# Performance work log

Measured on AMD Instinct MI355X. Metric: run time of the kernel, lower is better.

## Reference

```python
import jax, jax.numpy as jnp
import numpy as np
from jax import lax

B, DIM, H, W = 4, 192, 128, 128
NUM_HEADS = 4
EPS = 1e-12


def _conv1x1(x, w):
    # x: [b,c,h,w], w: [o,i,1,1]
    return lax.conv_general_dilated(x, w, (1, 1), 'VALID',
                                    dimension_numbers=('NCHW', 'OIHW', 'NCHW'))


def _dwconv3x3(x, w):
    # depthwise: w: [c,1,3,3], groups = c
    return lax.conv_general_dilated(x, w, (1, 1), ((1, 1), (1, 1)),
                                    dimension_numbers=('NCHW', 'OIHW', 'NCHW'),
                                    feature_group_count=w.shape[0])


def _l2norm(t):
    # normalize along last (spatial) axis, torch F.normalize semantics
    n = jnp.sqrt(jnp.sum(t * t, axis=-1, keepdims=True))
    return t / jnp.maximum(n, EPS)


def _heads(t, b, h, w):
    # [b, head*c, h, w] -> [b, head, c, h*w]
    return t.reshape(b, NUM_HEADS, t.shape[1] // NUM_HEADS, h * w)


def setup_inputs() -> dict:
    key = jax.random.key(0)
    ks = jax.random.split(key, 9)
    s = 0.02
    return {
        'x': jax.random.normal(ks[0], (B, DIM, H, W), jnp.float32),
        'ctx': jax.random.normal(ks[1], (B, DIM, H, W), jnp.float32),
        'x_qkv_w': jax.random.normal(ks[2], (DIM * 3, DIM, 1, 1), jnp.float32) * s,
        'x_dw_w': jax.random.normal(ks[3], (DIM * 3, 1, 3, 3), jnp.float32) * s,
        'x_po_w': jax.random.normal(ks[4], (DIM, DIM, 1, 1), jnp.float32) * s,
        'ctx_qkv_w': jax.random.normal(ks[5], (DIM * 3, DIM, 1, 1), jnp.float32) * s,
        'ctx_dw_w': jax.random.normal(ks[6], (DIM * 3, 1, 3, 3), jnp.float32) * s,
        'ctx_po_w': jax.random.normal(ks[7], (DIM, DIM, 1, 1), jnp.float32) * s,
        'temperature': jnp.ones((NUM_HEADS, 1, 1), jnp.float32),
    }


def reference(x, ctx, x_qkv_w, x_dw_w, x_po_w, ctx_qkv_w, ctx_dw_w, ctx_po_w, temperature):
    b, c, h, w = x.shape
    x_qkv = _dwconv3x3(_conv1x1(x, x_qkv_w), x_dw_w)
    x_q, x_k, x_v = jnp.split(x_qkv, 3, axis=1)
    ctx_qkv = _dwconv3x3(_conv1x1(ctx, ctx_qkv_w), ctx_dw_w)
    ctx_q, ctx_k, ctx_v = jnp.split(ctx_qkv, 3, axis=1)

    x_q, x_k, x_v = (_heads(t, b, h, w) for t in (x_q, x_k, x_v))
    ctx_q, ctx_k, ctx_v = (_heads(t, b, h, w) for t in (ctx_q, ctx_k, ctx_v))

    temp = temperature[None]  # [1, head, 1, 1]

    # ctx branch: x_q attends over ctx
    q1 = _l2norm(x_q)
    k1 = _l2norm(ctx_k)
    attn1 = jax.nn.softmax(jnp.einsum('bhcn,bhdn->bhcd', q1, k1) * temp, axis=-1)
    ctx_out = jnp.einsum('bhcd,bhdn->bhcn', attn1, ctx_v).reshape(b, c, h, w)
    ctx_out = _conv1x1(ctx_out, ctx_po_w)

    # x branch: ctx_q attends over x
    q2 = _l2norm(ctx_q)
    k2 = _l2norm(x_k)
    attn2 = jax.nn.softmax(jnp.einsum('bhcn,bhdn->bhcd', q2, k2) * temp, axis=-1)
    x_out = jnp.einsum('bhcd,bhdn->bhcn', attn2, x_v).reshape(b, c, h, w)
    x_out = _conv1x1(x_out, x_po_w)

    return (x_out, ctx_out)
```

## Files before the change

### kernel.cpp

```cpp
#include <hip/hip_runtime.h>
#include <hip/hip_bf16.h>

#define N_PIX 16384
#define W_ 128

typedef __attribute__((ext_vector_type(8))) unsigned short ushort8_t;
typedef __attribute__((ext_vector_type(4))) unsigned short ushort4_t;
typedef __attribute__((ext_vector_type(8))) __bf16 bf16x8;
typedef __attribute__((ext_vector_type(4))) float f32x4;

__device__ inline float bf2f(unsigned short u) {
    return __uint_as_float(((unsigned)u) << 16);
}
__device__ inline unsigned short f2bf(float f) {
    __hip_bfloat16 h = __float2bfloat16(f);
    return *(unsigned short*)&h;
}

__global__ __launch_bounds__(256) void k_pack_w(
    const float* __restrict__ wa, const float* __restrict__ wb,
    unsigned short* __restrict__ oa, unsigned short* __restrict__ ob)
{
    const int blk = blockIdx.x;
    const float* w = (blk < 108) ? wa : wb;
    unsigned short* o = (blk < 108) ? oa : ob;
    const int i = ((blk % 108) * 256 + threadIdx.x) * 4;
    float4 v = *(const float4*)(w + i);
    ushort4_t s;
    s[0] = f2bf(v.x); s[1] = f2bf(v.y); s[2] = f2bf(v.z); s[3] = f2bf(v.w);
    *(ushort4_t*)(o + i) = s;
}

__global__ __launch_bounds__(256, 2) void k_conv_mfma(
    const float* __restrict__ x, const float* __restrict__ ctx,
    const unsigned short* __restrict__ wx, const unsigned short* __restrict__ wc,
    unsigned short* __restrict__ ox, unsigned short* __restrict__ octx)
{
    const int p0 = blockIdx.x * 128;
    const int bb = blockIdx.y;
    const int b  = bb & 3;
    const bool isx = bb < 4;
    const float* inb = (isx ? x : ctx) + (long)b * 192 * N_PIX;
    const unsigned short* wbf = isx ? wx : wc;
    unsigned short* ob = (isx ? ox : octx) + (long)b * 576 * N_PIX;

    __shared__ unsigned short Xl[128 * 200];

    const int tid  = threadIdx.x;
    const int lane = tid & 63;
    const int wid  = tid >> 6;
    const int wo   = wid >> 1;
    const int wp   = wid & 1;
    const int l15  = lane & 15;
    const int lq   = lane >> 4;

    {
        const int p = tid & 127, kh = tid >> 7;
        #pragma unroll
        for (int seg = 0; seg < 12; seg++) {
            ushort8_t pk;
            #pragma unroll
            for (int j = 0; j < 8; j++)
                pk[j] = f2bf(inb[(long)(kh * 96 + seg * 8 + j) * N_PIX + p0 + p]);
            *(ushort8_t*)&Xl[p * 200 + kh * 96 + seg * 8] = pk;
        }
    }
    __syncthreads();

    #pragma unroll 1
    for (int oc = 0; oc < 6; oc++) {
        bf16x8 af[3][6];
        #pragma unroll
        for (int mt = 0; mt < 3; mt++)
            #pragma unroll
            for (int kc = 0; kc < 6; kc++)
                af[mt][kc] = *(const bf16x8*)(wbf +
                    (long)(oc * 96 + wo * 48 + mt * 16 + l15) * 192 + kc * 32 + lq * 8);

        f32x4 acc[3][4];
        const f32x4 zero = {0.f, 0.f, 0.f, 0.f};
        #pragma unroll
        for (int i = 0; i < 3; i++)
            #pragma unroll
            for (int j = 0; j < 4; j++) acc[i][j] = zero;

        #pragma unroll
        for (int kc = 0; kc < 6; kc++) {
            bf16x8 bfv[4];
            #pragma unroll
            for (int nt = 0; nt < 4; nt++)
                bfv[nt] = *(const bf16x8*)&Xl[(wp * 64 + nt * 16 + l15) * 200 + kc * 32 + lq * 8];
            #pragma unroll
            for (int mt = 0; mt < 3; mt++)
                #pragma unroll
                for (int nt = 0; nt < 4; nt++)
                    acc[mt][nt] = __builtin_amdgcn_mfma_f32_16x16x32_bf16(
                        af[mt][kc], bfv[nt], acc[mt][nt], 0, 0, 0);
        }
        #pragma unroll
        for (int mt = 0; mt < 3; mt++) {
            #pragma unroll
            for (int r = 0; r < 4; r++) {
                int o = oc * 96 + wo * 48 + mt * 16 + lq * 4 + r;
                long base = (long)o * N_PIX + p0 + wp * 64 + l15;
                #pragma unroll
                for (int nt = 0; nt < 4; nt++)
                    ob[base + nt * 16] = f2bf(acc[mt][nt][r]);
            }
        }
    }
}

__global__ __launch_bounds__(256) void k_dwconv(
    const unsigned short* __restrict__ tx, const unsigned short* __restrict__ tc,
    const float* __restrict__ wxd, const float* __restrict__ wcd,
    unsigned short* __restrict__ qx, unsigned short* __restrict__ qc)
{
    const int mz = blockIdx.y;
    const int br = (mz >= 2304) ? 1 : 0;
    const int m  = mz - br * 2304;
    const int ch = m % 576;
    const int y0 = blockIdx.x * 16;
    const unsigned short* ip = (br ? tc : tx) + (long)m * N_PIX;
    const float* wp = (br ? wcd : wxd) + ch * 9;
    unsigned short* op = (br ? qc : qx) + (long)m * N_PIX;

    __shared__ unsigned short Ll[18][136];

    const int tid = threadIdx.x;
    #pragma unroll
    for (int idx = tid; idx < 288; idx += 256) {
        int lr = idx >> 4, lc = (idx & 15) * 8;
        int gy = y0 - 1 + lr;
        ushort8_t v;
        #pragma unroll
        for (int j = 0; j < 8; j++) v[j] = 0;
        if ((unsigned)gy <= 127u)
            v = *(const ushort8_t*)(ip + gy * W_ + lc);
        *(ushort8_t*)&Ll[lr][lc] = v;
    }
    float wv[9];
    #pragma unroll
    for (int i = 0; i < 9; i++) wv[i] = wp[i];
    __syncthreads();

    const int r  = tid >> 4;
    const int xg = (tid & 15) * 8;

    float o[8];
    #pragma unroll
    for (int j = 0; j < 8; j++) o[j] = 0.f;

    #pragma unroll
    for (int dy = 0; dy < 3; dy++) {
        const unsigned short* lrow = &Ll[r + dy][0];
        float c[10];
        c[0] = (xg == 0) ? 0.f : bf2f(lrow[xg - 1]);
        ushort8_t mid = *(const ushort8_t*)&lrow[xg];
        #pragma unroll
        for (int j = 0; j < 8; j++) c[1 + j] = bf2f(mid[j]);
        c[9] = (xg == 120) ? 0.f : bf2f(lrow[xg + 8]);
        const float w0 = wv[dy * 3], w1 = wv[dy * 3 + 1], w2 = wv[dy * 3 + 2];
        #pragma unroll
        for (int j = 0; j < 8; j++)
            o[j] = fmaf(w0, c[j], fmaf(w1, c[j + 1], fmaf(w2, c[j + 2], o[j])));
    }
    ushort8_t res;
    #pragma unroll
    for (int j = 0; j < 8; j++) res[j] = f2bf(o[j]);
    *(ushort8_t*)(op + (y0 + r) * W_ + xg) = res;
}

__global__ __launch_bounds__(256) void k_gram_mfma(
    const unsigned short* __restrict__ qkv_x,
    const unsigned short* __restrict__ qkv_c,
    float* __restrict__ S, float* __restrict__ qn, float* __restrict__ kn)
{
    const int attn = blockIdx.z;
    const int bh   = blockIdx.y;
    const int b = bh >> 2, h = bh & 3;
    const unsigned short* qb =
        (attn == 0 ? qkv_x : qkv_c) + ((long)b * 576 + h * 48) * N_PIX;
    const unsigned short* kb =
        (attn == 0 ? qkv_c : qkv_x) + ((long)b * 576 + 192 + h * 48) * N_PIX;

    __shared__ float Sl[48 * 49];
    __shared__ float qnl[48], knl[48];

    const int tid = threadIdx.x;
    for (int i = tid; i < 48 * 49; i += 256) Sl[i] = 0.f;
    if (tid < 48) { qnl[tid] = 0.f; knl[tid] = 0.f; }
    __syncthreads();

    const int lane = tid & 63, wid = tid >> 6;
    const int l15 = lane & 15, lq = lane >> 4;
    const long nbase = (long)blockIdx.x * 1024 + wid * 256;

    f32x4 acc[3][3], aq[3], ak[3];
    const f32x4 zero = {0.f, 0.f, 0.f, 0.f};
    #pragma unroll
    for (int i = 0; i < 3; i++) {
        aq[i] = zero; ak[i] = zero;
        #pragma unroll
        for (int j = 0; j < 3; j++) acc[i][j] = zero;
    }

    for (int ks = 0; ks < 8; ks++) {
        const long ns = nbase + ks * 32;
        bf16x8 af[3], bfv[3];
        #pragma unroll
        for (int mt = 0; mt < 3; mt++)
            af[mt] = *(const bf16x8*)(qb + (long)(mt * 16 + l15) * N_PIX + ns + lq * 8);
        #pragma unroll
        for (int nt = 0; nt < 3; nt++)
            bfv[nt] = *(const bf16x8*)(kb + (long)(nt * 16 + l15) * N_PIX + ns + lq * 8);
        #pragma unroll
        for (int mt = 0; mt < 3; mt++)
            #pragma unroll
            for (int nt = 0; nt < 3; nt++)
                acc[mt][nt] = __builtin_amdgcn_mfma_f32_16x16x32_bf16(
                    af[mt], bfv[nt], acc[mt][nt], 0, 0, 0);
        #pragma unroll
        for (int mt = 0; mt < 3; mt++)
            aq[mt] = __builtin_amdgcn_mfma_f32_16x16x32_bf16(af[mt], af[mt], aq[mt], 0, 0, 0);
        #pragma unroll
        for (int nt = 0; nt < 3; nt++)
            ak[nt] = __builtin_amdgcn_mfma_f32_16x16x32_bf16(bfv[nt], bfv[nt], ak[nt], 0, 0, 0);
    }

    #pragma unroll
    for (int mt = 0; mt < 3; mt++)
        #pragma unroll
        for (int nt = 0; nt < 3; nt++)
            #pragma unroll
            for (int r = 0; r < 4; r++)
                atomicAdd(&Sl[(mt * 16 + lq * 4 + r) * 49 + nt * 16 + l15],
                          acc[mt][nt][r]);
    #pragma unroll
    for (int mt = 0; mt < 3; mt++)
        #pragma unroll
        for (int r = 0; r < 4; r++)
            if (l15 == lq * 4 + r) {
                atomicAdd(&qnl[mt * 16 + l15], aq[mt][r]);
                atomicAdd(&knl[mt * 16 + l15], ak[mt][r]);
            }
    __syncthreads();

    float* Sg = S + (long)(attn * 16 + bh) * 2304;
    float* qg = qn + (long)(attn * 16 + bh) * 48;
    float* kg = kn + (long)(attn * 16 + bh) * 48;
    for (int i = tid; i < 2304; i += 256) {
        int row = i / 48, col = i - row * 48;
        atomicAdd(&Sg[i], Sl[row * 49 + col]);
    }
    if (tid < 48) atomicAdd(&qg[tid], qnl[tid]);
    else if (tid < 96) atomicAdd(&kg[tid - 48], knl[tid - 48]);
}

__global__ __launch_bounds__(192) void k_softmax(
    const float* __restrict__ S, const float* __restrict__ qn,
    const float* __restrict__ kn, const float* __restrict__ temp,
    float* __restrict__ P)
{
    const int attn = blockIdx.x, b = blockIdx.y;
    const int r = threadIdx.x;
    const int h = r / 48, c = r % 48;
    const int bh = b * 4 + h;
    const float t = temp[h];
    const float* Srow = S + ((long)(attn * 16 + bh) * 48 + c) * 48;
    const float* knp  = kn + (long)(attn * 16 + bh) * 48;
    const float qc = fmaxf(sqrtf(qn[(long)(attn * 16 + bh) * 48 + c]), 1e-12f);
    float lg[48];
    float mx = -1e30f;
    #pragma unroll
    for (int d = 0; d < 48; d++) {
        float kd = fmaxf(sqrtf(knp[d]), 1e-12f);
        lg[d] = Srow[d] / (qc * kd) * t;
        mx = fmaxf(mx, lg[d]);
    }
    float sum = 0.f;
    #pragma unroll
    for (int d = 0; d < 48; d++) { lg[d] = __expf(lg[d] - mx); sum += lg[d]; }
    const float inv = 1.f / sum;
    float* Pp = P + (((long)(attn * 4 + b) * 4 + h) * 48 + c) * 48;
    #pragma unroll
    for (int d = 0; d < 48; d++) Pp[d] = lg[d] * inv;
}

__global__ __launch_bounds__(192) void k_w2(
    const float* __restrict__ P, const float* __restrict__ x_po,
    const float* __restrict__ ctx_po, unsigned short* __restrict__ W2)
{
    const int h = blockIdx.x, b = blockIdx.y, attn = blockIdx.z;
    const float* po = (attn == 0) ? ctx_po : x_po;
    __shared__ float Pl[48][48];
    const float* Pp = P + ((long)(attn * 4 + b) * 4 + h) * 2304;
    for (int it = 0; it < 12; it++) {
        int idx = it * 192 + threadIdx.x;
        Pl[idx / 48][idx % 48] = Pp[idx];
    }
    __syncthreads();
    const int o = threadIdx.x;
    float acc[48];
    #pragma unroll
    for (int d = 0; d < 48; d++) acc[d] = 0.f;
    for (int c = 0; c < 48; c++) {
        float pv = po[(long)o * 192 + h * 48 + c];
        #pragma unroll
        for (int d = 0; d < 48; d++)
            acc[d] = fmaf(pv, Pl[c][d], acc[d]);
    }
    unsigned short* wp = W2 + ((long)(attn * 4 + b) * 192 + o) * 192 + h * 48;
    #pragma unroll
    for (int d = 0; d < 48; d++) wp[d] = f2bf(acc[d]);
}

__global__ __launch_bounds__(256, 2) void k_gemm_v(
    const unsigned short* __restrict__ qkv_x,
    const unsigned short* __restrict__ qkv_c,
    const unsigned short* __restrict__ W2bf,
    float* __restrict__ out)
{
    const int p0 = blockIdx.x * 128;
    const int z  = blockIdx.y;
    const int br = z >> 2, b = z & 3;
    const unsigned short* v =
        (br == 0 ? qkv_x : qkv_c) + (long)b * 576 * N_PIX + 384L * N_PIX;
    const unsigned short* wb =
        W2bf + ((long)((br == 0 ? 1 : 0) * 4 + b)) * 36864;
    float* ob = out + (long)br * 12582912 + (long)b * 192 * N_PIX;

    __shared__ unsigned short Xl[128 * 200];

    const int tid  = threadIdx.x;
    const int lane = tid & 63;
    const int wid  = tid >> 6;
    const int wo   = wid >> 1;
    const int wp   = wid & 1;
    const int l15  = lane & 15;
    const int lq   = lane >> 4;

    {
        const int p = tid & 127, kh = tid >> 7;
        #pragma unroll
        for (int seg = 0; seg < 12; seg++) {
            ushort8_t pk;
            #pragma unroll
            for (int j = 0; j < 8; j++)
                pk[j] = v[(long)(kh * 96 + seg * 8 + j) * N_PIX + p0 + p];
            *(ushort8_t*)&Xl[p * 200 + kh * 96 + seg * 8] = pk;
        }
    }
    __syncthreads();

    #pragma unroll 1
    for (int oc = 0; oc < 2; oc++) {
        bf16x8 af[3][6];
        #pragma unroll
        for (int mt = 0; mt < 3; mt++)
            #pragma unroll
            for (int kc = 0; kc < 6; kc++)
                af[mt][kc] = *(const bf16x8*)(wb +
                    (long)(oc * 96 + wo * 48 + mt * 16 + l15) * 192 + kc * 32 + lq * 8);

        f32x4 acc[3][4];
        const f32x4 zero = {0.f, 0.f, 0.f, 0.f};
        #pragma unroll
        for (int i = 0; i < 3; i++)
            #pragma unroll
            for (int j = 0; j < 4; j++) acc[i][j] = zero;

        #pragma unroll
        for (int kc = 0; kc < 6; kc++) {
            bf16x8 bfv[4];
            #pragma unroll
            for (int nt = 0; nt < 4; nt++)
                bfv[nt] = *(const bf16x8*)&Xl[(wp * 64 + nt * 16 + l15) * 200 + kc * 32 + lq * 8];
            #pragma unroll
            for (int mt = 0; mt < 3; mt++)
                #pragma unroll
                for (int nt = 0; nt < 4; nt++)
                    acc[mt][nt] = __builtin_amdgcn_mfma_f32_16x16x32_bf16(
                        af[mt][kc], bfv[nt], acc[mt][nt], 0, 0, 0);
        }
        #pragma unroll
        for (int mt = 0; mt < 3; mt++) {
            #pragma unroll
            for (int r = 0; r < 4; r++) {
                int o = oc * 96 + wo * 48 + mt * 16 + lq * 4 + r;
                long base = (long)o * N_PIX + p0 + wp * 64 + l15;
                #pragma unroll
                for (int nt = 0; nt < 4; nt++)
                    ob[base + nt * 16] = acc[mt][nt][r];
            }
        }
    }
}

extern "C" void kernel_launch(void* const* d_in, const int* in_sizes, int n_in,
                              void* d_out, int out_size, void* d_ws, size_t ws_size,
                              hipStream_t stream) {
    (void)in_sizes; (void)n_in; (void)out_size;
    const float* x       = (const float*)d_in[0];
    const float* ctx     = (const float*)d_in[1];
    const float* x_qkv_w = (const float*)d_in[2];
    const float* x_dw_w  = (const float*)d_in[3];
    const float* x_po_w  = (const float*)d_in[4];
    const float* c_qkv_w = (const float*)d_in[5];
    const float* c_dw_w  = (const float*)d_in[6];
    const float* c_po_w  = (const float*)d_in[7];
    const float* temp    = (const float*)d_in[8];
    float* out = (float*)d_out;

    const long QKV = 37748736L;
    unsigned short* qkv_x16 = (unsigned short*)d_ws;
    unsigned short* qkv_c16 = qkv_x16 + QKV;
    float* S  = (float*)(qkv_c16 + QKV);
    float* qn = S + 73728;
    float* kn = qn + 1536;
    float* P  = kn + 1536;
    unsigned short* W2bf = (unsigned short*)(P + 73728);

    unsigned short* tmp_x = (unsigned short*)d_out;
    unsigned short* wx16  = (unsigned short*)d_out + QKV;
    unsigned short* wc16  = wx16 + 110592;

    k_pack_w<<<dim3(216), 256, 0, stream>>>(x_qkv_w, c_qkv_w, wx16, wc16);

    const size_t ws_needed = (size_t)QKV * 2 * 3;
    if (ws_size >= ws_needed) {
        unsigned short* tmp_c = (unsigned short*)S;
        k_conv_mfma<<<dim3(128, 8), 256, 0, stream>>>(
            x, ctx, wx16, wc16, tmp_x, tmp_c);
        k_dwconv<<<dim3(8, 4608), 256, 0, stream>>>(
            tmp_x, tmp_c, x_dw_w, c_dw_w, qkv_x16, qkv_c16);
    } else {
        k_conv_mfma<<<dim3(128, 4), 256, 0, stream>>>(
            x, x, wx16, wx16, tmp_x, tmp_x);
        k_dwconv<<<dim3(8, 2304), 256, 0, stream>>>(
            tmp_x, tmp_x, x_dw_w, x_dw_w, qkv_x16, qkv_x16);
        k_conv_mfma<<<dim3(128, 4), 256, 0, stream>>>(
            ctx, ctx, wc16, wc16, tmp_x, tmp_x);
        k_dwconv<<<dim3(8, 2304), 256, 0, stream>>>(
            tmp_x, tmp_x, c_dw_w, c_dw_w, qkv_c16, qkv_c16);
    }

    hipMemsetAsync(S, 0, (73728 + 1536 + 1536) * sizeof(float), stream);

    k_gram_mfma<<<dim3(16, 16, 2), 256, 0, stream>>>(qkv_x16, qkv_c16, S, qn, kn);
    k_softmax<<<dim3(2, 4), dim3(192), 0, stream>>>(S, qn, kn, temp, P);
    k_w2<<<dim3(4, 4, 2), dim3(192), 0, stream>>>(P, x_po_w, c_po_w, W2bf);

    k_gemm_v<<<dim3(128, 8), 256, 0, stream>>>(qkv_x16, qkv_c16, W2bf, out);
}
```

Baseline: 410.0 us.

## Stage conv weights in LDS with async double buffering; fuse softmax and W2

```diff
diff --git a/kernel.cpp b/kernel.cpp
--- a/kernel.cpp
+++ b/kernel.cpp
@@ -17,23 +17,33 @@
     return *(unsigned short*)&h;
 }
 
-__global__ __launch_bounds__(256) void k_pack_w(
+__device__ inline void glds16(const unsigned short* g, unsigned short* l) {
+    __builtin_amdgcn_global_load_lds(
+        (const __attribute__((address_space(1))) unsigned int*)g,
+        (__attribute__((address_space(3))) unsigned int*)l, 16, 0, 0);
+}
+
+__global__ __launch_bounds__(256) void k_pack_w_swz(
     const float* __restrict__ wa, const float* __restrict__ wb,
     unsigned short* __restrict__ oa, unsigned short* __restrict__ ob)
 {
     const int blk = blockIdx.x;
-    const float* w = (blk < 108) ? wa : wb;
-    unsigned short* o = (blk < 108) ? oa : ob;
-    const int i = ((blk % 108) * 256 + threadIdx.x) * 4;
-    float4 v = *(const float4*)(w + i);
-    ushort4_t s;
-    s[0] = f2bf(v.x); s[1] = f2bf(v.y); s[2] = f2bf(v.z); s[3] = f2bf(v.w);
-    *(ushort4_t*)(o + i) = s;
-}
-
-__global__ __launch_bounds__(256, 2) void k_conv_mfma(
+    const float* w = (blk < 54) ? wa : wb;
+    unsigned short* o = (blk < 54) ? oa : ob;
+    const int idx = (blk % 54) * 256 + threadIdx.x;
+    const int row = idx / 24, c = idx % 24;
+    const int sc = c ^ (row & 7);
+    const float* src = w + (long)row * 192 + c * 8;
+    ushort8_t s;
+    #pragma unroll
+    for (int j = 0; j < 8; j++) s[j] = f2bf(src[j]);
+    *(ushort8_t*)(o + (long)row * 192 + sc * 8) = s;
+}
+
+__global__ __launch_bounds__(256) void k_conv_mfma(
     const float* __restrict__ x, const float* __restrict__ ctx,
-    const unsigned short* __restrict__ wx, const unsigned short* __restrict__ wc,
+    const unsigned short* __restrict__ wx,
+    const unsigned short* __restrict__ wc,
     unsigned short* __restrict__ ox, unsigned short* __restrict__ octx)
 {
     const int p0 = blockIdx.x * 128;
@@ -41,10 +51,11 @@
     const int b  = bb & 3;
     const bool isx = bb < 4;
     const float* inb = (isx ? x : ctx) + (long)b * 192 * N_PIX;
-    const unsigned short* wbf = isx ? wx : wc;
+    const unsigned short* wswz = isx ? wx : wc;
     unsigned short* ob = (isx ? ox : octx) + (long)b * 576 * N_PIX;
 
     __shared__ unsigned short Xl[128 * 200];
+    __shared__ unsigned short Wl[2][96 * 192];
 
     const int tid  = threadIdx.x;
     const int lane = tid & 63;
@@ -55,6 +66,14 @@
     const int lq   = lane >> 4;
 
     {
+        const long cb = (long)wid * 9216;
+        #pragma unroll
+        for (int it = 0; it < 9; it++)
+            glds16(wswz + (cb + it * 1024) / 2 + lane * 8,
+                   &Wl[0][(cb + it * 1024) / 2]);
+    }
+
+    {
         const int p = tid & 127, kh = tid >> 7;
         #pragma unroll
         for (int seg = 0; seg < 12; seg++) {
@@ -69,14 +88,14 @@
 
     #pragma unroll 1
     for (int oc = 0; oc < 6; oc++) {
-        bf16x8 af[3][6];
-        #pragma unroll
-        for (int mt = 0; mt < 3; mt++)
-            #pragma unroll
-            for (int kc = 0; kc < 6; kc++)
-                af[mt][kc] = *(const bf16x8*)(wbf +
-                    (long)(oc * 96 + wo * 48 + mt * 16 + l15) * 192 + kc * 32 + lq * 8);
-
+        if (oc + 1 < 6) {
+            const long gb = (long)(oc + 1) * 36864 + (long)wid * 9216;
+            unsigned short* lb = &Wl[(oc + 1) & 1][wid * 4608];
+            #pragma unroll
+            for (int it = 0; it < 9; it++)
+                glds16(wswz + (gb + it * 1024) / 2 + lane * 8, lb + it * 512);
+        }
+        const unsigned short* Wb = Wl[oc & 1];
         f32x4 acc[3][4];
         const f32x4 zero = {0.f, 0.f, 0.f, 0.f};
         #pragma unroll
@@ -86,7 +105,13 @@
 
         #pragma unroll
         for (int kc = 0; kc < 6; kc++) {
-            bf16x8 bfv[4];
+            bf16x8 af[3], bfv[4];
+            #pragma unroll
+            for (int mt = 0; mt < 3; mt++) {
+                const int row = wo * 48 + mt * 16 + l15;
+                const int sc  = (kc * 4 + lq) ^ (l15 & 7);
+                af[mt] = *(const bf16x8*)&Wb[row * 192 + sc * 8];
+            }
             #pragma unroll
             for (int nt = 0; nt < 4; nt++)
                 bfv[nt] = *(const bf16x8*)&Xl[(wp * 64 + nt * 16 + l15) * 200 + kc * 32 + lq * 8];
@@ -95,7 +120,7 @@
                 #pragma unroll
                 for (int nt = 0; nt < 4; nt++)
                     acc[mt][nt] = __builtin_amdgcn_mfma_f32_16x16x32_bf16(
-                        af[mt][kc], bfv[nt], acc[mt][nt], 0, 0, 0);
+                        af[mt], bfv[nt], acc[mt][nt], 0, 0, 0);
         }
         #pragma unroll
         for (int mt = 0; mt < 3; mt++) {
@@ -108,6 +133,7 @@
                     ob[base + nt * 16] = f2bf(acc[mt][nt][r]);
             }
         }
+        __syncthreads();
     }
 }
 
@@ -257,65 +283,62 @@
     else if (tid < 96) atomicAdd(&kg[tid - 48], knl[tid - 48]);
 }
 
-__global__ __launch_bounds__(192) void k_softmax(
+__global__ __launch_bounds__(192) void k_sm_w2(
     const float* __restrict__ S, const float* __restrict__ qn,
     const float* __restrict__ kn, const float* __restrict__ temp,
-    float* __restrict__ P)
+    const float* __restrict__ x_po, const float* __restrict__ ctx_po,
+    unsigned short* __restrict__ W2)
 {
     const int attn = blockIdx.x, b = blockIdx.y;
-    const int r = threadIdx.x;
-    const int h = r / 48, c = r % 48;
-    const int bh = b * 4 + h;
-    const float t = temp[h];
-    const float* Srow = S + ((long)(attn * 16 + bh) * 48 + c) * 48;
-    const float* knp  = kn + (long)(attn * 16 + bh) * 48;
-    const float qc = fmaxf(sqrtf(qn[(long)(attn * 16 + bh) * 48 + c]), 1e-12f);
-    float lg[48];
-    float mx = -1e30f;
-    #pragma unroll
-    for (int d = 0; d < 48; d++) {
-        float kd = fmaxf(sqrtf(knp[d]), 1e-12f);
-        lg[d] = Srow[d] / (qc * kd) * t;
-        mx = fmaxf(mx, lg[d]);
-    }
-    float sum = 0.f;
-    #pragma unroll
-    for (int d = 0; d < 48; d++) { lg[d] = __expf(lg[d] - mx); sum += lg[d]; }
-    const float inv = 1.f / sum;
-    float* Pp = P + (((long)(attn * 4 + b) * 4 + h) * 48 + c) * 48;
-    #pragma unroll
-    for (int d = 0; d < 48; d++) Pp[d] = lg[d] * inv;
-}
-
-__global__ __launch_bounds__(192) void k_w2(
-    const float* __restrict__ P, const float* __restrict__ x_po,
-    const float* __restrict__ ctx_po, unsigned short* __restrict__ W2)
-{
-    const int h = blockIdx.x, b = blockIdx.y, attn = blockIdx.z;
-    const float* po = (attn == 0) ? ctx_po : x_po;
-    __shared__ float Pl[48][48];
-    const float* Pp = P + ((long)(attn * 4 + b) * 4 + h) * 2304;
-    for (int it = 0; it < 12; it++) {
-        int idx = it * 192 + threadIdx.x;
-        Pl[idx / 48][idx % 48] = Pp[idx];
-    }
-    __syncthreads();
-    const int o = threadIdx.x;
-    float acc[48];
-    #pragma unroll
-    for (int d = 0; d < 48; d++) acc[d] = 0.f;
-    for (int c = 0; c < 48; c++) {
-        float pv = po[(long)o * 192 + h * 48 + c];
-        #pragma unroll
-        for (int d = 0; d < 48; d++)
-            acc[d] = fmaf(pv, Pl[c][d], acc[d]);
-    }
-    unsigned short* wp = W2 + ((long)(attn * 4 + b) * 192 + o) * 192 + h * 48;
-    #pragma unroll
-    for (int d = 0; d < 48; d++) wp[d] = f2bf(acc[d]);
-}
-
-__global__ __launch_bounds__(256, 2) void k_gemm_v(
+    __shared__ float Pl[4][48][48];
+
+    {
+        const int r = threadIdx.x;
+        const int h = r / 48, c = r % 48;
+        const int bh = b * 4 + h;
+        const float t = temp[h];
+        const float* Srow = S + ((long)(attn * 16 + bh) * 48 + c) * 48;
+        const float* knp  = kn + (long)(attn * 16 + bh) * 48;
+        const float qc = fmaxf(sqrtf(qn[(long)(attn * 16 + bh) * 48 + c]), 1e-12f);
+        float lg[48];
+        float mx = -1e30f;
+        #pragma unroll
+        for (int d = 0; d < 48; d++) {
+            float kd = fmaxf(sqrtf(knp[d]), 1e-12f);
+            lg[d] = Srow[d] / (qc * kd) * t;
+            mx = fmaxf(mx, lg[d]);
+        }
+        float sum = 0.f;
+        #pragma unroll
+        for (int d = 0; d < 48; d++) { lg[d] = __expf(lg[d] - mx); sum += lg[d]; }
+        const float inv = 1.f / sum;
+        #pragma unroll
+        for (int d = 0; d < 48; d++) Pl[h][c][d] = lg[d] * inv;
+    }
+    __syncthreads();
+
+    {
+        const float* po = (attn == 0) ? ctx_po : x_po;
+        const int o = threadIdx.x;
+        unsigned short* wp = W2 + ((long)(attn * 4 + b) * 192 + o) * 192;
+        #pragma unroll 1
+        for (int h = 0; h < 4; h++) {
+            float acc[48];
+            #pragma unroll
+            for (int d = 0; d < 48; d++) acc[d] = 0.f;
+            for (int c = 0; c < 48; c++) {
+                float pv = po[(long)o * 192 + h * 48 + c];
+                #pragma unroll
+                for (int d = 0; d < 48; d++)
+                    acc[d] = fmaf(pv, Pl[h][c][d], acc[d]);
+            }
+            #pragma unroll
+            for (int d = 0; d < 48; d++) wp[h * 48 + d] = f2bf(acc[d]);
+        }
+    }
+}
+
+__global__ __launch_bounds__(256) void k_gemm_v(
     const unsigned short* __restrict__ qkv_x,
     const unsigned short* __restrict__ qkv_c,
     const unsigned short* __restrict__ W2bf,
@@ -418,14 +441,13 @@
     float* S  = (float*)(qkv_c16 + QKV);
     float* qn = S + 73728;
     float* kn = qn + 1536;
-    float* P  = kn + 1536;
-    unsigned short* W2bf = (unsigned short*)(P + 73728);
+    unsigned short* W2bf = (unsigned short*)(kn + 1536);
 
     unsigned short* tmp_x = (unsigned short*)d_out;
     unsigned short* wx16  = (unsigned short*)d_out + QKV;
     unsigned short* wc16  = wx16 + 110592;
 
-    k_pack_w<<<dim3(216), 256, 0, stream>>>(x_qkv_w, c_qkv_w, wx16, wc16);
+    k_pack_w_swz<<<dim3(108), 256, 0, stream>>>(x_qkv_w, c_qkv_w, wx16, wc16);
 
     const size_t ws_needed = (size_t)QKV * 2 * 3;
     if (ws_size >= ws_needed) {
@@ -448,8 +470,8 @@
     hipMemsetAsync(S, 0, (73728 + 1536 + 1536) * sizeof(float), stream);
 
     k_gram_mfma<<<dim3(16, 16, 2), 256, 0, stream>>>(qkv_x16, qkv_c16, S, qn, kn);
-    k_softmax<<<dim3(2, 4), dim3(192), 0, stream>>>(S, qn, kn, temp, P);
-    k_w2<<<dim3(4, 4, 2), dim3(192), 0, stream>>>(P, x_po_w, c_po_w, W2bf);
+    k_sm_w2<<<dim3(2, 4), dim3(192), 0, stream>>>(
+        S, qn, kn, temp, x_po_w, c_po_w, W2bf);
 
     k_gemm_v<<<dim3(128, 8), 256, 0, stream>>>(qkv_x16, qkv_c16, W2bf, out);
 }
```

Result: slower. 450.0 us (+9.8%).
